# Performance work log

Hardware: AMD Instinct MI355X
Metric: run time of the kernel (lower is better)

Reference implementation:

```python
import jax, jax.numpy as jnp
from jax import lax
import numpy as np

NEG = -10000.0

def sequence_mask(length, max_len):
    # [B, max_len] bool
    return jnp.arange(max_len)[None, :] < length[:, None]

def mdn_loss(logp, text_lengths, mel_lengths):
    # logp: [B, T_seq, T_mel]; CTC-style forward recursion over T_mel
    B, T_seq, T_mel = logp.shape
    init = jnp.full((B, T_seq), NEG, logp.dtype).at[:, 0].set(logp[:, 0, 0])
    logp_t = jnp.moveaxis(logp, 2, 0)  # [T_mel, B, T_seq]

    def step(alpha, lp):  # alpha: [B, T_seq]
        shifted = jnp.concatenate(
            [jnp.full((B, 1), NEG, alpha.dtype), alpha[:, :-1]], axis=1)
        new = jnp.logaddexp(alpha + 1e-4, shifted + 1e-4) + lp
        return new, new

    _, cols = lax.scan(step, init, logp_t[1:])
    log_alpha = jnp.concatenate([init[None], cols], axis=0)  # [T_mel, B, T_seq]
    alpha_last = log_alpha[mel_lengths - 1, jnp.arange(B), text_lengths - 1]
    return -alpha_last.mean() / T_seq

def mse_loss_masked(x, target, length):
    # seq_len_norm=False branch: sum of masked squared error / mask.sum() over expanded mask
    B, T, D = x.shape
    mask = sequence_mask(length, T)[:, :, None].astype(x.dtype)  # [B, T, 1]
    diff = x * mask - target * mask
    return jnp.sum(diff * diff) / (jnp.sum(mask) * D)

def sample_wise_min_max(x, mask):
    # x: [B, T, D], mask: [B, T, 1] bool; min/max over dims (1,2)
    maximum = jnp.max(jnp.where(mask, x, 0.0), axis=(1, 2), keepdims=True)
    minimum = jnp.min(jnp.where(mask, x, jnp.inf), axis=(1, 2), keepdims=True)
    return (x - minimum) / (maximum - minimum + 1e-8)

def _gaussian_kernel(size=11, sigma=1.5):
    coords = jnp.arange(size, dtype=jnp.float32) - (size - 1) / 2.0
    g = jnp.exp(-(coords ** 2) / (2.0 * sigma ** 2))
    g = g / g.sum()
    return jnp.outer(g, g)

def _ssim_mean(x, y):
    # x, y: [B, 1, H, W]; 11x11 gaussian SSIM, VALID conv, k1=0.01, k2=0.03, data_range=1
    k = _gaussian_kernel()[None, None].astype(x.dtype)  # [1,1,11,11]
    conv = lambda z: lax.conv_general_dilated(z, k, (1, 1), 'VALID')
    mu_x, mu_y = conv(x), conv(y)
    sxx = conv(x * x) - mu_x * mu_x
    syy = conv(y * y) - mu_y * mu_y
    sxy = conv(x * y) - mu_x * mu_y
    c1, c2 = 0.01 ** 2, 0.03 ** 2
    cs = (2.0 * sxy + c2) / (sxx + syy + c2)
    ssim_map = ((2.0 * mu_x * mu_y + c1) / (mu_x * mu_x + mu_y * mu_y + c1)) * cs
    return ssim_map.mean()

def ssim_loss(y_hat, y, length):
    mask = sequence_mask(length, y.shape[1])[:, :, None]  # [B, T, 1] bool
    y_norm = sample_wise_min_max(y, mask)
    y_hat_norm = sample_wise_min_max(y_hat, mask)
    m = mask.astype(y.dtype)
    loss = 1.0 - _ssim_mean((y_norm * m)[:, None], (y_hat_norm * m)[:, None])
    return jnp.clip(loss, 0.0, 1.0)

SSIM_ALPHA = 1.0
DUR_ALPHA = 1.0
SPEC_ALPHA = 1.0
MDN_ALPHA = 1.0

def setup_inputs() -> dict:
    key = jax.random.key(0)
    ks = jax.random.split(key, 8)
    B, T_seq, T_mel, D = 64, 256, 2048, 80
    logp = jax.random.normal(ks[0], (B, T_seq, T_mel), jnp.float32)
    decoder_output = jax.random.normal(ks[1], (B, T_mel, D), jnp.float32)
    decoder_target = jax.random.uniform(ks[2], (B, T_mel, D), jnp.float32)
    dur_output = jax.random.normal(ks[3], (B, T_seq), jnp.float32)
    dur_target = jax.random.uniform(ks[4], (B, T_seq), jnp.float32)
    decoder_output_lens = jax.random.randint(ks[5], (B,), T_mel // 2, T_mel + 1)
    input_lens = jax.random.randint(ks[6], (B,), T_seq // 2, T_seq + 1)
    return {
        'logp': logp,
        'decoder_output': decoder_output,
        'decoder_target': decoder_target,
        'dur_output': dur_output,
        'dur_target': dur_target,
        'decoder_output_lens': decoder_output_lens,
        'input_lens': input_lens,
        'phase': 4,
    }

def reference(logp, decoder_output, decoder_target, dur_output, dur_target,
              decoder_output_lens, input_lens, phase):
    spec_l = ssim_l = dur_l = mdn_l = 0.0
    if phase == 0:
        mdn_l = mdn_loss(logp, input_lens, decoder_output_lens)
    elif phase == 1:
        spec_l = mse_loss_masked(decoder_output, decoder_target, decoder_output_lens)
        ssim_l = ssim_loss(decoder_output, decoder_target, decoder_output_lens)
    elif phase == 2:
        mdn_l = mdn_loss(logp, input_lens, decoder_output_lens)
        spec_l = mse_loss_masked(decoder_output, decoder_target, decoder_output_lens)
        ssim_l = ssim_loss(decoder_output, decoder_target, decoder_output_lens)
    elif phase == 3:
        dur_l = mse_loss_masked(dur_output[:, :, None], dur_target[:, :, None], input_lens)
    else:
        mdn_l = mdn_loss(logp, input_lens, decoder_output_lens)
        spec_l = mse_loss_masked(decoder_output, decoder_target, decoder_output_lens)
        ssim_l = ssim_loss(decoder_output, decoder_target, decoder_output_lens)
        dur_l = mse_loss_masked(dur_output[:, :, None], dur_target[:, :, None], input_lens)
    loss = SPEC_ALPHA * spec_l + SSIM_ALPHA * ssim_l + DUR_ALPHA * dur_l + MDN_ALPHA * mdn_l
    return loss
```

## Files before the change

### kernel.cpp

```cpp
#include <hip/hip_runtime.h>
#include <math.h>

typedef unsigned short u16;
typedef unsigned int u32;

#define INV_LN2 1.44269504088896f
#define LN2     0.693147180559945f
#define NEG2    (-14426.9504f)


struct Ws {
  double ssim_sum;
  double dur_sum;
  double spec_part[256];
  float  mnT[256], mxT[256], mnO[256], mxO[256];
  float  A[64 * 256];
  float  Bv[64 * 256];
  float  ckF[64 * 256];
  float  ckB[64 * 256];
};

__device__ __forceinline__ float lse2f(float a, float b) {
  float m = fmaxf(a, b);
  float d = fabsf(a - b);
  return m + __builtin_amdgcn_logf(1.0f + __builtin_amdgcn_exp2f(-d));
}
__device__ __forceinline__ float lae2g(float a, float b, float g) {
  float m = fmaxf(a, b);
  float d = fabsf(a - b);
  return (m + g) + __builtin_amdgcn_logf(1.0f + __builtin_amdgcn_exp2f(-d));
}
__device__ __forceinline__ u16 bf16rn(float f) {
  u32 u = __float_as_uint(f);
  u32 r = (u + 0x7fffu + ((u >> 16) & 1u)) >> 16;
  return (u16)r;
}

constexpr float G11[11] = {
  0.00102838f, 0.00759876f, 0.03600077f, 0.10936070f, 0.21300554f,
  0.26601172f,
  0.21300554f, 0.10936070f, 0.03600077f, 0.00759876f, 0.00102838f};

#define TSTR 264
#define TSZ  (32 * TSTR)

__device__ __forceinline__ void stage_tile(const float* __restrict__ gb, int kb,
                                           u16* dst, int tid) {
  const int ltid = tid - 64;
  const int tb = kb << 5;
#pragma unroll
  for (int it = 0; it < 11; ++it) {
    int i = ltid + it * 192;
    if (i < 2048) {
      int s = i >> 3, e = i & 7;
      float4 v = *(const float4*)(gb + (size_t)s * 2048 + tb + 4 * e);
      u16* d = dst + (4 * e) * TSTR + s;
      d[0]        = bf16rn(v.x * INV_LN2);
      d[TSTR]     = bf16rn(v.y * INV_LN2);
      d[2 * TSTR] = bf16rn(v.z * INV_LN2);
      d[3 * TSTR] = bf16rn(v.w * INV_LN2);
    }
  }
}

__global__ __launch_bounds__(256) void kseg1(
    const float* __restrict__ logp,
    const float* __restrict__ deco, const float* __restrict__ dect,
    const float* __restrict__ duro, const float* __restrict__ durt,
    const int* __restrict__ mel_lens, const int* __restrict__ inp_lens,
    Ws* __restrict__ ws) {
  __shared__ u16 TB[2 * TSZ];
  __shared__ float L[5][4];
  const int bid = blockIdx.x, tid = threadIdx.x;
  const int l = tid;

  if (bid < 64) {
    const int b = bid;
    const float* gb = logp + (size_t)b * 256 * 2048;
    float a0 = NEG2, a1 = NEG2, a2 = NEG2, a3 = NEG2;
    if (tid < 64 && l == 0) a0 = gb[0] * INV_LN2;
    auto FWD = [&](uint2 fg) {
      float g0 = __uint_as_float(fg.x << 16);
      float g1 = __uint_as_float(fg.x & 0xffff0000u);
      float g2 = __uint_as_float(fg.y << 16);
      float g3 = __uint_as_float(fg.y & 0xffff0000u);
      int up = __builtin_amdgcn_update_dpp(
          __float_as_int(NEG2), __float_as_int(a3), 0x138, 0xF, 0xF, false);
      float am1 = __int_as_float(up);
      float n0 = lae2g(a0, am1, g0);
      float n1 = lae2g(a1, a0, g1);
      float n2 = lae2g(a2, a1, g2);
      float n3 = lae2g(a3, a2, g3);
      a0 = n0; a1 = n1; a2 = n2; a3 = n3;
    };
    if (tid >= 64) stage_tile(gb, 0, TB, tid);
    __syncthreads();
    if (tid >= 64) stage_tile(gb, 1, TB + TSZ, tid);
    else {
      const u16* fs = TB + 4 * l;
      for (int i = 1; i < 32; ++i) FWD(*(const uint2*)(fs + i * TSTR));
    }
    __syncthreads();
    for (int j = 1; j < 16; ++j) {
      if (tid >= 64) {
        if (j < 15) stage_tile(gb, j + 1, TB + ((j + 1) & 1) * TSZ, tid);
      } else {
        __builtin_amdgcn_s_setprio(1);
        const u16* fs = TB + (j & 1) * TSZ + 4 * l;
        uint2 fb[2][4];
#pragma unroll
        for (int k = 0; k < 4; ++k) fb[0][k] = *(const uint2*)(fs + k * TSTR);
#pragma unroll
        for (int g = 0; g < 8; ++g) {
          const int cur = g & 1, nxt = cur ^ 1;
          if (g < 7) {
#pragma unroll
            for (int k = 0; k < 4; ++k)
              fb[nxt][k] = *(const uint2*)(fs + ((g + 1) * 4 + k) * TSTR);
          }
#pragma unroll
          for (int k = 0; k < 4; ++k) FWD(fb[cur][k]);
        }
        __builtin_amdgcn_s_setprio(0);
      }
      __syncthreads();
    }
    if (tid < 64)
      *(float4*)&ws->ckF[b * 256 + 4 * l] = make_float4(a0, a1, a2, a3);
    return;
  }

  if (bid < 128) {
    const int b = bid - 64;
    const int T = mel_lens[b] - 1;
    const int ss = inp_lens[b] - 1;
    const int kbT = T >> 5;
    const float* gb = logp + (size_t)b * 256 * 2048;
    float b0 = NEG2, b1 = NEG2, b2 = NEG2, b3 = NEG2;
    if (tid < 64) {
      b0 = (4 * l + 0 == ss) ? 0.f : NEG2;
      b1 = (4 * l + 1 == ss) ? 0.f : NEG2;
      b2 = (4 * l + 2 == ss) ? 0.f : NEG2;
      b3 = (4 * l + 3 == ss) ? 0.f : NEG2;
    }
    auto BWD = [&](uint2 bg, bool act) {
      float g0 = __uint_as_float(bg.x << 16);
      float g1 = __uint_as_float(bg.x & 0xffff0000u);
      float g2 = __uint_as_float(bg.y << 16);
      float g3 = __uint_as_float(bg.y & 0xffff0000u);
      float c0 = b0 + g0, c1 = b1 + g1, c2 = b2 + g2, c3 = b3 + g3;
      int dn = __builtin_amdgcn_update_dpp(
          __float_as_int(NEG2), __float_as_int(c0), 0x130, 0xF, 0xF, false);
      float cp = __int_as_float(dn);
      float m0 = lse2f(c0, c1);
      float m1 = lse2f(c1, c2);
      float m2 = lse2f(c2, c3);
      float m3 = lse2f(c3, cp);
      b0 = act ? m0 : b0; b1 = act ? m1 : b1;
      b2 = act ? m2 : b2; b3 = act ? m3 : b3;
    };
    if (tid >= 64) { if (kbT >= 32) stage_tile(gb, kbT, TB, tid); }
    __syncthreads();
    if (tid >= 64) {
      if (kbT - 1 >= 32) stage_tile(gb, kbT - 1, TB + TSZ, tid);
    } else if (kbT >= 32) {
      const u16* bs = TB + 4 * l;
      for (int ii = 31; ii >= 0; --ii) {
        int tt = (kbT << 5) + ii;
        if (tt <= T) BWD(*(const uint2*)(bs + ii * TSTR), true);
      }
    }
    __syncthreads();
    for (int j = 1; j < 16; ++j) {
      if (tid >= 64) {
        int bk = kbT - j - 1;
        if (j < 15 && bk >= 32) stage_tile(gb, bk, TB + ((j + 1) & 1) * TSZ, tid);
      } else {
        __builtin_amdgcn_s_setprio(1);
        const u16* bs = TB + (j & 1) * TSZ + 4 * l;
        const bool act = (kbT - j) >= 32;
        uint2 bb[2][4];
#pragma unroll
        for (int k = 0; k < 4; ++k) bb[0][k] = *(const uint2*)(bs + (31 - k) * TSTR);
#pragma unroll
        for (int g = 0; g < 8; ++g) {
          const int cur = g & 1, nxt = cur ^ 1;
          if (g < 7) {
#pragma unroll
            for (int k = 0; k < 4; ++k)
              bb[nxt][k] = *(const uint2*)(bs + (31 - ((g + 1) * 4 + k)) * TSTR);
          }
#pragma unroll
          for (int k = 0; k < 4; ++k) BWD(bb[cur][k], act);
        }
        __builtin_amdgcn_s_setprio(0);
      }
      __syncthreads();
    }
    if (tid < 64)
      *(float4*)&ws->ckB[b * 256 + 4 * l] = make_float4(b0, b1, b2, b3);
    return;
  }

  if (bid < 384) {
    int idx = bid - 128, b = idx >> 2, part = idx & 3;
    int len = mel_lens[b];
    int rbeg = part * 512;
    int rcnt = len - rbeg; rcnt = rcnt < 0 ? 0 : (rcnt > 512 ? 512 : rcnt);
    float mnT = __builtin_inff(), mxT = -__builtin_inff();
    float mnO = __builtin_inff(), mxO = -__builtin_inff();
    float ssum = 0.f;
    if (rcnt > 0) {
      const float4* po = (const float4*)(deco + ((size_t)(b * 2048 + rbeg)) * 80);
      const float4* pt = (const float4*)(dect + ((size_t)(b * 2048 + rbeg)) * 80);
      int n4 = rcnt * 20;
      for (int i = tid; i < n4; i += 256) {
        float4 vo = po[i], vt = pt[i];
        mnO = fminf(mnO, fminf(fminf(vo.x, vo.y), fminf(vo.z, vo.w)));
        mxO = fmaxf(mxO, fmaxf(fmaxf(vo.x, vo.y), fmaxf(vo.z, vo.w)));
        mnT = fminf(mnT, fminf(fminf(vt.x, vt.y), fminf(vt.z, vt.w)));
        mxT = fmaxf(mxT, fmaxf(fmaxf(vt.x, vt.y), fmaxf(vt.z, vt.w)));
        float dx = vo.x - vt.x, dy = vo.y - vt.y, dz = vo.z - vt.z, dw = vo.w - vt.w;
        ssum += dx * dx + dy * dy + dz * dz + dw * dw;
      }
    }
    for (int o = 32; o; o >>= 1) {
      mnT = fminf(mnT, __shfl_xor(mnT, o));
      mxT = fmaxf(mxT, __shfl_xor(mxT, o));
      mnO = fminf(mnO, __shfl_xor(mnO, o));
      mxO = fmaxf(mxO, __shfl_xor(mxO, o));
      ssum += __shfl_xor(ssum, o);
    }
    int w = tid >> 6;
    if ((tid & 63) == 0) { L[0][w] = mnT; L[1][w] = mxT; L[2][w] = mnO; L[3][w] = mxO; L[4][w] = ssum; }
    __syncthreads();
    if (tid == 0) {
      mnT = fminf(fminf(L[0][0], L[0][1]), fminf(L[0][2], L[0][3]));
      mxT = fmaxf(fmaxf(L[1][0], L[1][1]), fmaxf(L[1][2], L[1][3]));
      mnO = fminf(fminf(L[2][0], L[2][1]), fminf(L[2][2], L[2][3]));
      mxO = fmaxf(fmaxf(L[3][0], L[3][1]), fmaxf(L[3][2], L[3][3]));
      ssum = L[4][0] + L[4][1] + L[4][2] + L[4][3];
      ws->mnT[idx] = mnT; ws->mxT[idx] = mxT; ws->mnO[idx] = mnO; ws->mxO[idx] = mxO;
      ws->spec_part[idx] = (double)ssum;
    }
    return;
  }

  {
    float ssum = 0.f;
    for (int i = tid; i < 64 * 256; i += 256) {
      int b2 = i >> 8, s2 = i & 255;
      if (s2 < inp_lens[b2]) { float d = duro[i] - durt[i]; ssum += d * d; }
    }
    for (int o = 32; o; o >>= 1) ssum += __shfl_xor(ssum, o);
    int w = tid >> 6;
    if ((tid & 63) == 0) L[4][w] = ssum;
    __syncthreads();
    if (tid == 0) {
      ws->dur_sum = (double)(L[4][0] + L[4][1] + L[4][2] + L[4][3]);
      ws->ssim_sum = 0.0;
    }
  }
}

__global__ __launch_bounds__(512) void kseg2(
    const float* __restrict__ logp,
    const float* __restrict__ deco, const float* __restrict__ dect,
    const int* __restrict__ mel_lens, const int* __restrict__ inp_lens,
    Ws* __restrict__ ws) {
  __shared__ float SMF[14712];
  const int bid = blockIdx.x, tid = threadIdx.x;
  const int l = tid;
  u16* TB = (u16*)SMF;

  if (bid < 64) {
    const int b = bid;
    const float* gb = logp + (size_t)b * 256 * 2048;
    float a0 = NEG2, a1 = NEG2, a2 = NEG2, a3 = NEG2;
    if (tid < 64) {
      float4 c = *(const float4*)&ws->ckF[b * 256 + 4 * l];
      a0 = c.x; a1 = c.y; a2 = c.z; a3 = c.w;
    }
    auto FWD = [&](uint2 fg) {
      float g0 = __uint_as_float(fg.x << 16);
      float g1 = __uint_as_float(fg.x & 0xffff0000u);
      float g2 = __uint_as_float(fg.y << 16);
      float g3 = __uint_as_float(fg.y & 0xffff0000u);
      int up = __builtin_amdgcn_update_dpp(
          __float_as_int(NEG2), __float_as_int(a3), 0x138, 0xF, 0xF, false);
      float am1 = __int_as_float(up);
      float n0 = lae2g(a0, am1, g0);
      float n1 = lae2g(a1, a0, g1);
      float n2 = lae2g(a2, a1, g2);
      float n3 = lae2g(a3, a2, g3);
      a0 = n0; a1 = n1; a2 = n2; a3 = n3;
    };
    if (tid >= 64 && tid < 256) stage_tile(gb, 16, TB, tid);
    __syncthreads();
    for (int j = 16; j < 32; ++j) {
      if (tid >= 64 && tid < 256) {
        if (j < 31) stage_tile(gb, j + 1, TB + ((j + 1) & 1) * TSZ, tid);
      } else if (tid < 64) {
        __builtin_amdgcn_s_setprio(1);
        const u16* fs = TB + (j & 1) * TSZ + 4 * l;
        uint2 fb[2][4];
#pragma unroll
        for (int k = 0; k < 4; ++k) fb[0][k] = *(const uint2*)(fs + k * TSTR);
#pragma unroll
        for (int g = 0; g < 8; ++g) {
          const int cur = g & 1, nxt = cur ^ 1;
          if (g < 7) {
#pragma unroll
            for (int k = 0; k < 4; ++k)
              fb[nxt][k] = *(const uint2*)(fs + ((g + 1) * 4 + k) * TSTR);
          }
#pragma unroll
          for (int k = 0; k < 4; ++k) FWD(fb[cur][k]);
        }
        __builtin_amdgcn_s_setprio(0);
      }
      __syncthreads();
    }
    if (tid < 64)
      *(float4*)&ws->A[b * 256 + 4 * l] = make_float4(a0, a1, a2, a3);
    return;
  }

  if (bid < 128) {
    const int b = bid - 64;
    const int T = mel_lens[b] - 1;
    const int kbT = T >> 5;
    float b0 = NEG2, b1 = NEG2, b2 = NEG2, b3 = NEG2;
    if (tid < 64) {
      float4 c = *(const float4*)&ws->ckB[b * 256 + 4 * l];
      b0 = c.x; b1 = c.y; b2 = c.z; b3 = c.w;
    }
    if (kbT - 16 < 32) {
      if (tid < 64)
        *(float4*)&ws->Bv[b * 256 + 4 * l] = make_float4(b0, b1, b2, b3);
      return;
    }
    const float* gb = logp + (size_t)b * 256 * 2048;
    auto BWD = [&](uint2 bg, bool act) {
      float g0 = __uint_as_float(bg.x << 16);
      float g1 = __uint_as_float(bg.x & 0xffff0000u);
      float g2 = __uint_as_float(bg.y << 16);
      float g3 = __uint_as_float(bg.y & 0xffff0000u);
      float c0 = b0 + g0, c1 = b1 + g1, c2 = b2 + g2, c3 = b3 + g3;
      int dn = __builtin_amdgcn_update_dpp(
          __float_as_int(NEG2), __float_as_int(c0), 0x130, 0xF, 0xF, false);
      float cp = __int_as_float(dn);
      float m0 = lse2f(c0, c1);
      float m1 = lse2f(c1, c2);
      float m2 = lse2f(c2, c3);
      float m3 = lse2f(c3, cp);
      b0 = act ? m0 : b0; b1 = act ? m1 : b1;
      b2 = act ? m2 : b2; b3 = act ? m3 : b3;
    };
    if (tid >= 64 && tid < 256) stage_tile(gb, kbT - 16, TB, tid);
    __syncthreads();
    for (int j = 16; j < 32; ++j) {
      if (tid >= 64 && tid < 256) {
        int bk = kbT - j - 1;
        if (j < 31 && bk >= 32) stage_tile(gb, bk, TB + ((j + 1) & 1) * TSZ, tid);
      } else if (tid < 64) {
        __builtin_amdgcn_s_setprio(1);
        const u16* bs = TB + (j & 1) * TSZ + 4 * l;
        const bool act = (kbT - j) >= 32;
        uint2 bb[2][4];
#pragma unroll
        for (int k = 0; k < 4; ++k) bb[0][k] = *(const uint2*)(bs + (31 - k) * TSTR);
#pragma unroll
        for (int g = 0; g < 8; ++g) {
          const int cur = g & 1, nxt = cur ^ 1;
          if (g < 7) {
#pragma unroll
            for (int k = 0; k < 4; ++k)
              bb[nxt][k] = *(const uint2*)(bs + (31 - ((g + 1) * 4 + k)) * TSTR);
          }
#pragma unroll
          for (int k = 0; k < 4; ++k) BWD(bb[cur][k], act);
        }
        __builtin_amdgcn_s_setprio(0);
      }
      __syncthreads();
    }
    if (tid < 64)
      *(float4*)&ws->Bv[b * 256 + 4 * l] = make_float4(b0, b1, b2, b3);
    return;
  }

  float* cc = SMF;
  float* R = SMF + 14700;
  int cix = bid - 128;
  int b = cix >> 6, tile = cix & 63;
  int r0 = tile * 32;
  int nrows = 2038 - r0; nrows = nrows > 32 ? 32 : nrows;
  int nin = nrows + 10;
  int len = mel_lens[b];

  if (r0 >= len) {
    if (tid == 0) atomicAdd(&ws->ssim_sum, (double)(nrows * 70));
    return;
  }

  float mnT = fminf(fminf(ws->mnT[4 * b], ws->mnT[4 * b + 1]), fminf(ws->mnT[4 * b + 2], ws->mnT[4 * b + 3]));
  float mxT = fmaxf(fmaxf(ws->mxT[4 * b], ws->mxT[4 * b + 1]), fmaxf(ws->mxT[4 * b + 2], ws->mxT[4 * b + 3]));
  float mnO = fminf(fminf(ws->mnO[4 * b], ws->mnO[4 * b + 1]), fminf(ws->mnO[4 * b + 2], ws->mnO[4 * b + 3]));
  float mxO = fmaxf(fmaxf(ws->mxO[4 * b], ws->mxO[4 * b + 1]), fmaxf(ws->mxO[4 * b + 2], ws->mxO[4 * b + 3]));
  if (len < 2048) { mxT = fmaxf(mxT, 0.f); mxO = fmaxf(mxO, 0.f); }
  float sT = 1.0f / (mxT - mnT + 1e-8f);
  float sO = 1.0f / (mxO - mnO + 1e-8f);
  const float* po = deco + (size_t)b * 2048 * 80;
  const float* pt = dect + (size_t)b * 2048 * 80;

  for (int task = tid; task < nin * 18; task += 512) {
    int r = task / 18, q = task - 18 * r;
    int j0 = q * 4;
    int grow = r0 + r;
    float sacc[4][5];
#pragma unroll
    for (int e = 0; e < 4; ++e)
#pragma unroll
      for (int c = 0; c < 5; ++c) sacc[e][c] = 0.f;
    if (grow < len) {
      const float* rowt = pt + (size_t)grow * 80 + j0;
      const float* rowo = po + (size_t)grow * 80 + j0;
      float ft[16], fo[16];
      *(float4*)&ft[0]  = *(const float4*)(rowt);
      *(float4*)&ft[4]  = *(const float4*)(rowt + 4);
      *(float4*)&ft[8]  = *(const float4*)(rowt + 8);
      *(float4*)&ft[12] = (j0 == 68) ? *(const float4*)(rowt + 8)
                                     : *(const float4*)(rowt + 12);
      *(float4*)&fo[0]  = *(const float4*)(rowo);
      *(float4*)&fo[4]  = *(const float4*)(rowo + 4);
      *(float4*)&fo[8]  = *(const float4*)(rowo + 8);
      *(float4*)&fo[12] = (j0 == 68) ? *(const float4*)(rowo + 8)
                                     : *(const float4*)(rowo + 12);
#pragma unroll
      for (int i = 0; i < 16; ++i) {
        ft[i] = (ft[i] - mnT) * sT;
        fo[i] = (fo[i] - mnO) * sO;
      }
#pragma unroll
      for (int e = 0; e < 4; ++e) {
#pragma unroll
        for (int k = 0; k < 11; ++k) {
          float tn = ft[e + k], on = fo[e + k], g = G11[k];
          sacc[e][0] = fmaf(g, tn, sacc[e][0]);
          sacc[e][1] = fmaf(g, on, sacc[e][1]);
          sacc[e][2] = fmaf(g * tn, tn, sacc[e][2]);
          sacc[e][3] = fmaf(g * on, on, sacc[e][3]);
          sacc[e][4] = fmaf(g * on, tn, sacc[e][4]);
        }
      }
    }
    int base = r * 70 + j0;
#pragma unroll
    for (int c = 0; c < 5; ++c) {
      *(float2*)&cc[c * 2940 + base] = make_float2(sacc[0][c], sacc[1][c]);
      if (j0 < 68)
        *(float2*)&cc[c * 2940 + base + 2] = make_float2(sacc[2][c], sacc[3][c]);
    }
  }
  __syncthreads();

  float acc = 0.f;
  for (int q2 = tid; q2 < nrows * 70; q2 += 512) {
    int i = q2 / 70, j = q2 - 70 * i;
    float mx = 0, my = 0, xx = 0, yy = 0, xy = 0;
#pragma unroll
    for (int k = 0; k < 11; ++k) {
      float g = G11[k];
      int o = (i + k) * 70 + j;
      mx = fmaf(g, cc[o], mx);
      my = fmaf(g, cc[2940 + o], my);
      xx = fmaf(g, cc[2 * 2940 + o], xx);
      yy = fmaf(g, cc[3 * 2940 + o], yy);
      xy = fmaf(g, cc[4 * 2940 + o], xy);
    }
    float vx = xx - mx * mx, vy = yy - my * my, vxy = xy - mx * my;
    float cs = (2.f * vxy + 9e-4f) / (vx + vy + 9e-4f);
    float lum = (2.f * mx * my + 1e-4f) / (mx * mx + my * my + 1e-4f);
    acc += lum * cs;
  }
  for (int o = 32; o; o >>= 1) acc += __shfl_xor(acc, o);
  if ((tid & 63) == 0) R[tid >> 6] = acc;
  __syncthreads();
  if (tid == 0)
    atomicAdd(&ws->ssim_sum,
              (double)(R[0] + R[1] + R[2] + R[3] + R[4] + R[5] + R[6] + R[7]));
}

__global__ __launch_bounds__(256) void kfin(
    const int* __restrict__ mel_lens, const int* __restrict__ inp_lens,
    Ws* __restrict__ ws, float* __restrict__ out) {
  __shared__ float MD[64];
  __shared__ double LD[4][4];
  int tid = threadIdx.x;
  {
    int b = tid >> 2, q = tid & 3;
    const float* Ab = ws->A + b * 256;
    const float* Bb = ws->Bv + b * 256;
    float mx = -3.0e38f;
    for (int j = q; j < 256; j += 4) mx = fmaxf(mx, Ab[j] + Bb[j]);
    mx = fmaxf(mx, __shfl_xor(mx, 1));
    mx = fmaxf(mx, __shfl_xor(mx, 2));
    float se = 0.f;
    for (int j = q; j < 256; j += 4)
      se += __builtin_amdgcn_exp2f(Ab[j] + Bb[j] - mx);
    se += __shfl_xor(se, 1);
    se += __shfl_xor(se, 2);
    if (q == 0)
      MD[b] = LN2 * (mx + __builtin_amdgcn_logf(se)) + (float)(mel_lens[b] - 1) * 1e-4f;
  }
  __syncthreads();
  double sp = ws->spec_part[tid];
  double md = 0.0, ml = 0.0, il = 0.0;
  if (tid < 64) {
    md = (double)MD[tid];
    ml = (double)mel_lens[tid];
    il = (double)inp_lens[tid];
  }
  for (int o = 32; o; o >>= 1) {
    sp += __shfl_xor(sp, o);
    md += __shfl_xor(md, o);
    ml += __shfl_xor(ml, o);
    il += __shfl_xor(il, o);
  }
  int w = tid >> 6;
  if ((tid & 63) == 0) { LD[w][0] = sp; LD[w][1] = md; LD[w][2] = ml; LD[w][3] = il; }
  __syncthreads();
  if (tid == 0) {
    sp = LD[0][0] + LD[1][0] + LD[2][0] + LD[3][0];
    md = LD[0][1] + LD[1][1] + LD[2][1] + LD[3][1];
    ml = LD[0][2] + LD[1][2] + LD[2][2] + LD[3][2];
    il = LD[0][3] + LD[1][3] + LD[2][3] + LD[3][3];
    double spec = sp / (ml * 80.0);
    double dur = ws->dur_sum / il;
    double mdn = -(md / 64.0) / 256.0;
    double sm = ws->ssim_sum / (64.0 * 2038.0 * 70.0);
    double sl = 1.0 - sm;
    sl = sl < 0.0 ? 0.0 : (sl > 1.0 ? 1.0 : sl);
    out[0] = (float)(spec + sl + dur + mdn);
  }
}

extern "C" void kernel_launch(void* const* d_in, const int* in_sizes, int n_in,
                              void* d_out, int out_size, void* d_ws, size_t ws_size,
                              hipStream_t stream) {
  const float* logp = (const float*)d_in[0];
  const float* deco = (const float*)d_in[1];
  const float* dect = (const float*)d_in[2];
  const float* duro = (const float*)d_in[3];
  const float* durt = (const float*)d_in[4];
  const int* mel_lens = (const int*)d_in[5];
  const int* inp_lens = (const int*)d_in[6];
  Ws* ws = (Ws*)d_ws;
  hipLaunchKernelGGL(kseg1, dim3(385), dim3(256), 0, stream,
                     logp, deco, dect, duro, durt, mel_lens, inp_lens, ws);
  hipLaunchKernelGGL(kseg2, dim3(128 + 64 * 64), dim3(512), 0, stream,
                     logp, deco, dect, mel_lens, inp_lens, ws);
  hipLaunchKernelGGL(kfin, dim3(1), dim3(256), 0, stream,
                     mel_lens, inp_lens, ws, (float*)d_out);
}
```

Before: 178.8 us.

## Split SSIM conv tiles across both recursion kernels via new prologue reduction kernel

The min/max and MSE reductions move into a new small kernel k0 that runs first. Half of the SSIM convolution tiles (the even indices) now run inside kseg1 next to the first MDN recursion segment, and the other half stay in kseg2. kseg1 grows to 512 threads, and only threads below 256 take part in the recursion and staging. The aim is to fill idle CUs during the latency-bound serial recursion blocks with SSIM work, at the cost of an extra kernel launch and larger blocks for kseg1.

```diff
diff --git a/kernel.cpp b/kernel.cpp
--- a/kernel.cpp
+++ b/kernel.cpp
@@ -63,16 +63,188 @@
   }
 }
 
-__global__ __launch_bounds__(256) void kseg1(
-    const float* __restrict__ logp,
+__global__ __launch_bounds__(256) void k0(
     const float* __restrict__ deco, const float* __restrict__ dect,
     const float* __restrict__ duro, const float* __restrict__ durt,
     const int* __restrict__ mel_lens, const int* __restrict__ inp_lens,
     Ws* __restrict__ ws) {
-  __shared__ u16 TB[2 * TSZ];
   __shared__ float L[5][4];
   const int bid = blockIdx.x, tid = threadIdx.x;
+
+  if (bid < 256) {
+    int idx = bid, b = idx >> 2, part = idx & 3;
+    int len = mel_lens[b];
+    int rbeg = part * 512;
+    int rcnt = len - rbeg; rcnt = rcnt < 0 ? 0 : (rcnt > 512 ? 512 : rcnt);
+    float mnT = __builtin_inff(), mxT = -__builtin_inff();
+    float mnO = __builtin_inff(), mxO = -__builtin_inff();
+    float ssum = 0.f;
+    if (rcnt > 0) {
+      const float4* po = (const float4*)(deco + ((size_t)(b * 2048 + rbeg)) * 80);
+      const float4* pt = (const float4*)(dect + ((size_t)(b * 2048 + rbeg)) * 80);
+      int n4 = rcnt * 20;
+      for (int i = tid; i < n4; i += 256) {
+        float4 vo = po[i], vt = pt[i];
+        mnO = fminf(mnO, fminf(fminf(vo.x, vo.y), fminf(vo.z, vo.w)));
+        mxO = fmaxf(mxO, fmaxf(fmaxf(vo.x, vo.y), fmaxf(vo.z, vo.w)));
+        mnT = fminf(mnT, fminf(fminf(vt.x, vt.y), fminf(vt.z, vt.w)));
+        mxT = fmaxf(mxT, fmaxf(fmaxf(vt.x, vt.y), fmaxf(vt.z, vt.w)));
+        float dx = vo.x - vt.x, dy = vo.y - vt.y, dz = vo.z - vt.z, dw = vo.w - vt.w;
+        ssum += dx * dx + dy * dy + dz * dz + dw * dw;
+      }
+    }
+    for (int o = 32; o; o >>= 1) {
+      mnT = fminf(mnT, __shfl_xor(mnT, o));
+      mxT = fmaxf(mxT, __shfl_xor(mxT, o));
+      mnO = fminf(mnO, __shfl_xor(mnO, o));
+      mxO = fmaxf(mxO, __shfl_xor(mxO, o));
+      ssum += __shfl_xor(ssum, o);
+    }
+    int w = tid >> 6;
+    if ((tid & 63) == 0) { L[0][w] = mnT; L[1][w] = mxT; L[2][w] = mnO; L[3][w] = mxO; L[4][w] = ssum; }
+    __syncthreads();
+    if (tid == 0) {
+      mnT = fminf(fminf(L[0][0], L[0][1]), fminf(L[0][2], L[0][3]));
+      mxT = fmaxf(fmaxf(L[1][0], L[1][1]), fmaxf(L[1][2], L[1][3]));
+      mnO = fminf(fminf(L[2][0], L[2][1]), fminf(L[2][2], L[2][3]));
+      mxO = fmaxf(fmaxf(L[3][0], L[3][1]), fmaxf(L[3][2], L[3][3]));
+      ssum = L[4][0] + L[4][1] + L[4][2] + L[4][3];
+      ws->mnT[idx] = mnT; ws->mxT[idx] = mxT; ws->mnO[idx] = mnO; ws->mxO[idx] = mxO;
+      ws->spec_part[idx] = (double)ssum;
+    }
+    return;
+  }
+
+  {
+    float ssum = 0.f;
+    for (int i = tid; i < 64 * 256; i += 256) {
+      int b2 = i >> 8, s2 = i & 255;
+      if (s2 < inp_lens[b2]) { float d = duro[i] - durt[i]; ssum += d * d; }
+    }
+    for (int o = 32; o; o >>= 1) ssum += __shfl_xor(ssum, o);
+    int w = tid >> 6;
+    if ((tid & 63) == 0) L[4][w] = ssum;
+    __syncthreads();
+    if (tid == 0) {
+      ws->dur_sum = (double)(L[4][0] + L[4][1] + L[4][2] + L[4][3]);
+      ws->ssim_sum = 0.0;
+    }
+  }
+}
+
+__device__ __forceinline__ void conv_tile(
+    int gci, const float* __restrict__ deco, const float* __restrict__ dect,
+    const int* __restrict__ mel_lens, Ws* __restrict__ ws, float* SMF, int tid) {
+  float* cc = SMF;
+  float* R = SMF + 14700;
+  int b = gci >> 6, tile = gci & 63;
+  int r0 = tile * 32;
+  int nrows = 2038 - r0; nrows = nrows > 32 ? 32 : nrows;
+  int nin = nrows + 10;
+  int len = mel_lens[b];
+
+  if (r0 >= len) {
+    if (tid == 0) atomicAdd(&ws->ssim_sum, (double)(nrows * 70));
+    return;
+  }
+
+  float mnT = fminf(fminf(ws->mnT[4 * b], ws->mnT[4 * b + 1]), fminf(ws->mnT[4 * b + 2], ws->mnT[4 * b + 3]));
+  float mxT = fmaxf(fmaxf(ws->mxT[4 * b], ws->mxT[4 * b + 1]), fmaxf(ws->mxT[4 * b + 2], ws->mxT[4 * b + 3]));
+  float mnO = fminf(fminf(ws->mnO[4 * b], ws->mnO[4 * b + 1]), fminf(ws->mnO[4 * b + 2], ws->mnO[4 * b + 3]));
+  float mxO = fmaxf(fmaxf(ws->mxO[4 * b], ws->mxO[4 * b + 1]), fmaxf(ws->mxO[4 * b + 2], ws->mxO[4 * b + 3]));
+  if (len < 2048) { mxT = fmaxf(mxT, 0.f); mxO = fmaxf(mxO, 0.f); }
+  float sT = 1.0f / (mxT - mnT + 1e-8f);
+  float sO = 1.0f / (mxO - mnO + 1e-8f);
+  const float* po = deco + (size_t)b * 2048 * 80;
+  const float* pt = dect + (size_t)b * 2048 * 80;
+
+  for (int task = tid; task < nin * 18; task += 512) {
+    int r = task / 18, q = task - 18 * r;
+    int j0 = q * 4;
+    int grow = r0 + r;
+    float sacc[4][5];
+#pragma unroll
+    for (int e = 0; e < 4; ++e)
+#pragma unroll
+      for (int c = 0; c < 5; ++c) sacc[e][c] = 0.f;
+    if (grow < len) {
+      const float* rowt = pt + (size_t)grow * 80 + j0;
+      const float* rowo = po + (size_t)grow * 80 + j0;
+      float ft[16], fo[16];
+      *(float4*)&ft[0]  = *(const float4*)(rowt);
+      *(float4*)&ft[4]  = *(const float4*)(rowt + 4);
+      *(float4*)&ft[8]  = *(const float4*)(rowt + 8);
+      *(float4*)&ft[12] = (j0 == 68) ? *(const float4*)(rowt + 8)
+                                     : *(const float4*)(rowt + 12);
+      *(float4*)&fo[0]  = *(const float4*)(rowo);
+      *(float4*)&fo[4]  = *(const float4*)(rowo + 4);
+      *(float4*)&fo[8]  = *(const float4*)(rowo + 8);
+      *(float4*)&fo[12] = (j0 == 68) ? *(const float4*)(rowo + 8)
+                                     : *(const float4*)(rowo + 12);
+#pragma unroll
+      for (int i = 0; i < 16; ++i) {
+        ft[i] = (ft[i] - mnT) * sT;
+        fo[i] = (fo[i] - mnO) * sO;
+      }
+#pragma unroll
+      for (int e = 0; e < 4; ++e) {
+#pragma unroll
+        for (int k = 0; k < 11; ++k) {
+          float tn = ft[e + k], on = fo[e + k], g = G11[k];
+          sacc[e][0] = fmaf(g, tn, sacc[e][0]);
+          sacc[e][1] = fmaf(g, on, sacc[e][1]);
+          sacc[e][2] = fmaf(g * tn, tn, sacc[e][2]);
+          sacc[e][3] = fmaf(g * on, on, sacc[e][3]);
+          sacc[e][4] = fmaf(g * on, tn, sacc[e][4]);
+        }
+      }
+    }
+    int base = r * 70 + j0;
+#pragma unroll
+    for (int c = 0; c < 5; ++c) {
+      *(float2*)&cc[c * 2940 + base] = make_float2(sacc[0][c], sacc[1][c]);
+      if (j0 < 68)
+        *(float2*)&cc[c * 2940 + base + 2] = make_float2(sacc[2][c], sacc[3][c]);
+    }
+  }
+  __syncthreads();
+
+  float acc = 0.f;
+  for (int q2 = tid; q2 < nrows * 70; q2 += 512) {
+    int i = q2 / 70, j = q2 - 70 * i;
+    float mx = 0, my = 0, xx = 0, yy = 0, xy = 0;
+#pragma unroll
+    for (int k = 0; k < 11; ++k) {
+      float g = G11[k];
+      int o = (i + k) * 70 + j;
+      mx = fmaf(g, cc[o], mx);
+      my = fmaf(g, cc[2940 + o], my);
+      xx = fmaf(g, cc[2 * 2940 + o], xx);
+      yy = fmaf(g, cc[3 * 2940 + o], yy);
+      xy = fmaf(g, cc[4 * 2940 + o], xy);
+    }
+    float vx = xx - mx * mx, vy = yy - my * my, vxy = xy - mx * my;
+    float cs = (2.f * vxy + 9e-4f) / (vx + vy + 9e-4f);
+    float lum = (2.f * mx * my + 1e-4f) / (mx * mx + my * my + 1e-4f);
+    acc += lum * cs;
+  }
+  for (int o = 32; o; o >>= 1) acc += __shfl_xor(acc, o);
+  if ((tid & 63) == 0) R[tid >> 6] = acc;
+  __syncthreads();
+  if (tid == 0)
+    atomicAdd(&ws->ssim_sum,
+              (double)(R[0] + R[1] + R[2] + R[3] + R[4] + R[5] + R[6] + R[7]));
+}
+
+__global__ __launch_bounds__(512) void kseg1(
+    const float* __restrict__ logp,
+    const float* __restrict__ deco, const float* __restrict__ dect,
+    const int* __restrict__ mel_lens, const int* __restrict__ inp_lens,
+    Ws* __restrict__ ws) {
+  __shared__ float SMF[14712];
+  const int bid = blockIdx.x, tid = threadIdx.x;
   const int l = tid;
+  u16* TB = (u16*)SMF;
 
   if (bid < 64) {
     const int b = bid;
@@ -93,18 +265,18 @@
       float n3 = lae2g(a3, a2, g3);
       a0 = n0; a1 = n1; a2 = n2; a3 = n3;
     };
-    if (tid >= 64) stage_tile(gb, 0, TB, tid);
-    __syncthreads();
-    if (tid >= 64) stage_tile(gb, 1, TB + TSZ, tid);
-    else {
+    if (tid >= 64 && tid < 256) stage_tile(gb, 0, TB, tid);
+    __syncthreads();
+    if (tid >= 64 && tid < 256) stage_tile(gb, 1, TB + TSZ, tid);
+    else if (tid < 64) {
       const u16* fs = TB + 4 * l;
       for (int i = 1; i < 32; ++i) FWD(*(const uint2*)(fs + i * TSTR));
     }
     __syncthreads();
     for (int j = 1; j < 16; ++j) {
-      if (tid >= 64) {
+      if (tid >= 64 && tid < 256) {
         if (j < 15) stage_tile(gb, j + 1, TB + ((j + 1) & 1) * TSZ, tid);
-      } else {
+      } else if (tid < 64) {
         __builtin_amdgcn_s_setprio(1);
         const u16* fs = TB + (j & 1) * TSZ + 4 * l;
         uint2 fb[2][4];
@@ -159,11 +331,11 @@
       b0 = act ? m0 : b0; b1 = act ? m1 : b1;
       b2 = act ? m2 : b2; b3 = act ? m3 : b3;
     };
-    if (tid >= 64) { if (kbT >= 32) stage_tile(gb, kbT, TB, tid); }
-    __syncthreads();
-    if (tid >= 64) {
+    if (tid >= 64 && tid < 256) { if (kbT >= 32) stage_tile(gb, kbT, TB, tid); }
+    __syncthreads();
+    if (tid >= 64 && tid < 256) {
       if (kbT - 1 >= 32) stage_tile(gb, kbT - 1, TB + TSZ, tid);
-    } else if (kbT >= 32) {
+    } else if (tid < 64 && kbT >= 32) {
       const u16* bs = TB + 4 * l;
       for (int ii = 31; ii >= 0; --ii) {
         int tt = (kbT << 5) + ii;
@@ -172,10 +344,10 @@
     }
     __syncthreads();
     for (int j = 1; j < 16; ++j) {
-      if (tid >= 64) {
+      if (tid >= 64 && tid < 256) {
         int bk = kbT - j - 1;
         if (j < 15 && bk >= 32) stage_tile(gb, bk, TB + ((j + 1) & 1) * TSZ, tid);
-      } else {
+      } else if (tid < 64) {
         __builtin_amdgcn_s_setprio(1);
         const u16* bs = TB + (j & 1) * TSZ + 4 * l;
         const bool act = (kbT - j) >= 32;
@@ -202,65 +374,7 @@
     return;
   }
 
-  if (bid < 384) {
-    int idx = bid - 128, b = idx >> 2, part = idx & 3;
-    int len = mel_lens[b];
-    int rbeg = part * 512;
-    int rcnt = len - rbeg; rcnt = rcnt < 0 ? 0 : (rcnt > 512 ? 512 : rcnt);
-    float mnT = __builtin_inff(), mxT = -__builtin_inff();
-    float mnO = __builtin_inff(), mxO = -__builtin_inff();
-    float ssum = 0.f;
-    if (rcnt > 0) {
-      const float4* po = (const float4*)(deco + ((size_t)(b * 2048 + rbeg)) * 80);
-      const float4* pt = (const float4*)(dect + ((size_t)(b * 2048 + rbeg)) * 80);
-      int n4 = rcnt * 20;
-      for (int i = tid; i < n4; i += 256) {
-        float4 vo = po[i], vt = pt[i];
-        mnO = fminf(mnO, fminf(fminf(vo.x, vo.y), fminf(vo.z, vo.w)));
-        mxO = fmaxf(mxO, fmaxf(fmaxf(vo.x, vo.y), fmaxf(vo.z, vo.w)));
-        mnT = fminf(mnT, fminf(fminf(vt.x, vt.y), fminf(vt.z, vt.w)));
-        mxT = fmaxf(mxT, fmaxf(fmaxf(vt.x, vt.y), fmaxf(vt.z, vt.w)));
-        float dx = vo.x - vt.x, dy = vo.y - vt.y, dz = vo.z - vt.z, dw = vo.w - vt.w;
-        ssum += dx * dx + dy * dy + dz * dz + dw * dw;
-      }
-    }
-    for (int o = 32; o; o >>= 1) {
-      mnT = fminf(mnT, __shfl_xor(mnT, o));
-      mxT = fmaxf(mxT, __shfl_xor(mxT, o));
-      mnO = fminf(mnO, __shfl_xor(mnO, o));
-      mxO = fmaxf(mxO, __shfl_xor(mxO, o));
-      ssum += __shfl_xor(ssum, o);
-    }
-    int w = tid >> 6;
-    if ((tid & 63) == 0) { L[0][w] = mnT; L[1][w] = mxT; L[2][w] = mnO; L[3][w] = mxO; L[4][w] = ssum; }
-    __syncthreads();
-    if (tid == 0) {
-      mnT = fminf(fminf(L[0][0], L[0][1]), fminf(L[0][2], L[0][3]));
-      mxT = fmaxf(fmaxf(L[1][0], L[1][1]), fmaxf(L[1][2], L[1][3]));
-      mnO = fminf(fminf(L[2][0], L[2][1]), fminf(L[2][2], L[2][3]));
-      mxO = fmaxf(fmaxf(L[3][0], L[3][1]), fmaxf(L[3][2], L[3][3]));
-      ssum = L[4][0] + L[4][1] + L[4][2] + L[4][3];
-      ws->mnT[idx] = mnT; ws->mxT[idx] = mxT; ws->mnO[idx] = mnO; ws->mxO[idx] = mxO;
-      ws->spec_part[idx] = (double)ssum;
-    }
-    return;
-  }
-
-  {
-    float ssum = 0.f;
-    for (int i = tid; i < 64 * 256; i += 256) {
-      int b2 = i >> 8, s2 = i & 255;
-      if (s2 < inp_lens[b2]) { float d = duro[i] - durt[i]; ssum += d * d; }
-    }
-    for (int o = 32; o; o >>= 1) ssum += __shfl_xor(ssum, o);
-    int w = tid >> 6;
-    if ((tid & 63) == 0) L[4][w] = ssum;
-    __syncthreads();
-    if (tid == 0) {
-      ws->dur_sum = (double)(L[4][0] + L[4][1] + L[4][2] + L[4][3]);
-      ws->ssim_sum = 0.0;
-    }
-  }
+  conv_tile((bid - 128) * 2, deco, dect, mel_lens, ws, SMF, tid);
 }
 
 __global__ __launch_bounds__(512) void kseg2(
@@ -390,106 +504,7 @@
     return;
   }
 
-  float* cc = SMF;
-  float* R = SMF + 14700;
-  int cix = bid - 128;
-  int b = cix >> 6, tile = cix & 63;
-  int r0 = tile * 32;
-  int nrows = 2038 - r0; nrows = nrows > 32 ? 32 : nrows;
-  int nin = nrows + 10;
-  int len = mel_lens[b];
-
-  if (r0 >= len) {
-    if (tid == 0) atomicAdd(&ws->ssim_sum, (double)(nrows * 70));
-    return;
-  }
-
-  float mnT = fminf(fminf(ws->mnT[4 * b], ws->mnT[4 * b + 1]), fminf(ws->mnT[4 * b + 2], ws->mnT[4 * b + 3]));
-  float mxT = fmaxf(fmaxf(ws->mxT[4 * b], ws->mxT[4 * b + 1]), fmaxf(ws->mxT[4 * b + 2], ws->mxT[4 * b + 3]));
-  float mnO = fminf(fminf(ws->mnO[4 * b], ws->mnO[4 * b + 1]), fminf(ws->mnO[4 * b + 2], ws->mnO[4 * b + 3]));
-  float mxO = fmaxf(fmaxf(ws->mxO[4 * b], ws->mxO[4 * b + 1]), fmaxf(ws->mxO[4 * b + 2], ws->mxO[4 * b + 3]));
-  if (len < 2048) { mxT = fmaxf(mxT, 0.f); mxO = fmaxf(mxO, 0.f); }
-  float sT = 1.0f / (mxT - mnT + 1e-8f);
-  float sO = 1.0f / (mxO - mnO + 1e-8f);
-  const float* po = deco + (size_t)b * 2048 * 80;
-  const float* pt = dect + (size_t)b * 2048 * 80;
-
-  for (int task = tid; task < nin * 18; task += 512) {
-    int r = task / 18, q = task - 18 * r;
-    int j0 = q * 4;
-    int grow = r0 + r;
-    float sacc[4][5];
-#pragma unroll
-    for (int e = 0; e < 4; ++e)
-#pragma unroll
-      for (int c = 0; c < 5; ++c) sacc[e][c] = 0.f;
-    if (grow < len) {
-      const float* rowt = pt + (size_t)grow * 80 + j0;
-      const float* rowo = po + (size_t)grow * 80 + j0;
-      float ft[16], fo[16];
-      *(float4*)&ft[0]  = *(const float4*)(rowt);
-      *(float4*)&ft[4]  = *(const float4*)(rowt + 4);
-      *(float4*)&ft[8]  = *(const float4*)(rowt + 8);
-      *(float4*)&ft[12] = (j0 == 68) ? *(const float4*)(rowt + 8)
-                                     : *(const float4*)(rowt + 12);
-      *(float4*)&fo[0]  = *(const float4*)(rowo);
-      *(float4*)&fo[4]  = *(const float4*)(rowo + 4);
-      *(float4*)&fo[8]  = *(const float4*)(rowo + 8);
-      *(float4*)&fo[12] = (j0 == 68) ? *(const float4*)(rowo + 8)
-                                     : *(const float4*)(rowo + 12);
-#pragma unroll
-      for (int i = 0; i < 16; ++i) {
-        ft[i] = (ft[i] - mnT) * sT;
-        fo[i] = (fo[i] - mnO) * sO;
-      }
-#pragma unroll
-      for (int e = 0; e < 4; ++e) {
-#pragma unroll
-        for (int k = 0; k < 11; ++k) {
-          float tn = ft[e + k], on = fo[e + k], g = G11[k];
-          sacc[e][0] = fmaf(g, tn, sacc[e][0]);
-          sacc[e][1] = fmaf(g, on, sacc[e][1]);
-          sacc[e][2] = fmaf(g * tn, tn, sacc[e][2]);
-          sacc[e][3] = fmaf(g * on, on, sacc[e][3]);
-          sacc[e][4] = fmaf(g * on, tn, sacc[e][4]);
-        }
-      }
-    }
-    int base = r * 70 + j0;
-#pragma unroll
-    for (int c = 0; c < 5; ++c) {
-      *(float2*)&cc[c * 2940 + base] = make_float2(sacc[0][c], sacc[1][c]);
-      if (j0 < 68)
-        *(float2*)&cc[c * 2940 + base + 2] = make_float2(sacc[2][c], sacc[3][c]);
-    }
-  }
-  __syncthreads();
-
-  float acc = 0.f;
-  for (int q2 = tid; q2 < nrows * 70; q2 += 512) {
-    int i = q2 / 70, j = q2 - 70 * i;
-    float mx = 0, my = 0, xx = 0, yy = 0, xy = 0;
-#pragma unroll
-    for (int k = 0; k < 11; ++k) {
-      float g = G11[k];
-      int o = (i + k) * 70 + j;
-      mx = fmaf(g, cc[o], mx);
-      my = fmaf(g, cc[2940 + o], my);
-      xx = fmaf(g, cc[2 * 2940 + o], xx);
-      yy = fmaf(g, cc[3 * 2940 + o], yy);
-      xy = fmaf(g, cc[4 * 2940 + o], xy);
-    }
-    float vx = xx - mx * mx, vy = yy - my * my, vxy = xy - mx * my;
-    float cs = (2.f * vxy + 9e-4f) / (vx + vy + 9e-4f);
-    float lum = (2.f * mx * my + 1e-4f) / (mx * mx + my * my + 1e-4f);
-    acc += lum * cs;
-  }
-  for (int o = 32; o; o >>= 1) acc += __shfl_xor(acc, o);
-  if ((tid & 63) == 0) R[tid >> 6] = acc;
-  __syncthreads();
-  if (tid == 0)
-    atomicAdd(&ws->ssim_sum,
-              (double)(R[0] + R[1] + R[2] + R[3] + R[4] + R[5] + R[6] + R[7]));
+  conv_tile((bid - 128) * 2 + 1, deco, dect, mel_lens, ws, SMF, tid);
 }
 
 __global__ __launch_bounds__(256) void kfin(
@@ -557,9 +572,11 @@
   const int* mel_lens = (const int*)d_in[5];
   const int* inp_lens = (const int*)d_in[6];
   Ws* ws = (Ws*)d_ws;
-  hipLaunchKernelGGL(kseg1, dim3(385), dim3(256), 0, stream,
-                     logp, deco, dect, duro, durt, mel_lens, inp_lens, ws);
-  hipLaunchKernelGGL(kseg2, dim3(128 + 64 * 64), dim3(512), 0, stream,
+  hipLaunchKernelGGL(k0, dim3(257), dim3(256), 0, stream,
+                     deco, dect, duro, durt, mel_lens, inp_lens, ws);
+  hipLaunchKernelGGL(kseg1, dim3(128 + 2048), dim3(512), 0, stream,
+                     logp, deco, dect, mel_lens, inp_lens, ws);
+  hipLaunchKernelGGL(kseg2, dim3(128 + 2048), dim3(512), 0, stream,
                      logp, deco, dect, mel_lens, inp_lens, ws);
   hipLaunchKernelGGL(kfin, dim3(1), dim3(256), 0, stream,
                      mel_lens, inp_lens, ws, (float*)d_out);
```

Result: faster. 157.4 us, median of 2 (-12.0%).
